# Kernel optimization log

Measured on AMD Instinct MI355X. Metric: run time of the kernel, lower is better.

Reference implementation:

```python
import jax, jax.numpy as jnp
import numpy as np

B, S, D_MODEL, H, D_KV = 2, 2048, 1024, 16, 64
NUM_BUCKETS, MAX_DIST = 32, 128


def _relative_position_bucket(rel_pos, num_buckets=NUM_BUCKETS, max_distance=MAX_DIST):
    # bidirectional (encoder) bucketing, matching T5Attention._relative_position_bucket
    nb = num_buckets // 2
    buckets = (rel_pos > 0).astype(jnp.int32) * nb
    rel = jnp.abs(rel_pos)
    max_exact = nb // 2
    is_small = rel < max_exact
    rel_f = jnp.maximum(rel.astype(jnp.float32), 1.0)  # guard log(0); masked by is_small anyway
    large = max_exact + (
        jnp.log(rel_f / max_exact) / np.log(max_distance / max_exact) * (nb - max_exact)
    ).astype(jnp.int32)
    large = jnp.minimum(large, nb - 1)
    return buckets + jnp.where(is_small, rel, large)


def setup_inputs() -> dict:
    key = jax.random.key(0)
    ks = jax.random.split(key, 6)
    sc = 1.0 / np.sqrt(D_MODEL)
    return {
        "hidden_states": jax.random.normal(ks[0], (B, S, D_MODEL), jnp.float32),
        "Wq": jax.random.normal(ks[1], (D_MODEL, H * D_KV), jnp.float32) * sc,
        "Wk": jax.random.normal(ks[2], (D_MODEL, H * D_KV), jnp.float32) * sc,
        "Wv": jax.random.normal(ks[3], (D_MODEL, H * D_KV), jnp.float32) * sc,
        "Wo": jax.random.normal(ks[4], (H * D_KV, D_MODEL), jnp.float32) * sc,
        "rel_bias_table": jax.random.normal(ks[5], (NUM_BUCKETS, H), jnp.float32),
    }


def reference(hidden_states, Wq, Wk, Wv, Wo, rel_bias_table):
    b, s, _ = hidden_states.shape
    # projections (T5 uses no bias, scale=1.0 in attention)
    q = (hidden_states @ Wq).reshape(b, s, H, D_KV).transpose(0, 2, 1, 3)  # bhsd
    k = (hidden_states @ Wk).reshape(b, s, H, D_KV).transpose(0, 2, 1, 3)
    v = (hidden_states @ Wv).reshape(b, s, H, D_KV).transpose(0, 2, 1, 3)

    # relative position bias: [1, H, S, S]
    ctx = jnp.arange(s)[:, None]
    mem = jnp.arange(s)[None, :]
    buckets = _relative_position_bucket(mem - ctx)          # [S, S]
    pos_bias = rel_bias_table[buckets]                       # [S, S, H]
    pos_bias = pos_bias.transpose(2, 0, 1)[None]             # [1, H, S, S]

    scores = jnp.einsum("bhqd,bhkd->bhqk", q, k) + pos_bias  # scale = 1.0
    probs = jax.nn.softmax(scores, axis=-1)
    attn = jnp.einsum("bhqk,bhkd->bhqd", probs, v)
    attn = attn.transpose(0, 2, 1, 3).reshape(b, s, H * D_KV)
    return attn @ Wo
```

## Files before the change

### kernel.cpp

```cpp
#include <hip/hip_runtime.h>
#include <hip/hip_fp16.h>

#define S_LEN 2048
#define NH 16
#define DK 64
#define DM 1024
#define NB 2
#define QKV_SZ (NB * NH * S_LEN * DK)

typedef _Float16 half8 __attribute__((ext_vector_type(8)));
typedef _Float16 half4v __attribute__((ext_vector_type(4)));
typedef __fp16 fp16x2 __attribute__((ext_vector_type(2)));
typedef float f32x4 __attribute__((ext_vector_type(4)));

static __device__ __forceinline__ half4v pack4(const f32x4 v) {
  fp16x2 lo = __builtin_amdgcn_cvt_pkrtz(v[0], v[1]);
  fp16x2 hi = __builtin_amdgcn_cvt_pkrtz(v[2], v[3]);
  half4v r;
  ((fp16x2*)&r)[0] = lo;
  ((fp16x2*)&r)[1] = hi;
  return r;
}

#define GLL(gp, lp)                                                              \
  __builtin_amdgcn_global_load_lds(                                              \
      (const __attribute__((address_space(1))) unsigned int*)(gp),               \
      (__attribute__((address_space(3))) unsigned int*)(lp), 16, 0, 0)


__global__ __launch_bounds__(256) void conv_f32_f16(const float* __restrict__ in,
                                                    _Float16* __restrict__ out, int n4) {
  int i = blockIdx.x * 256 + threadIdx.x;
  if (i >= n4) return;
  float4 v = ((const float4*)in)[i];
  half4v o;
  o[0] = (_Float16)v.x; o[1] = (_Float16)v.y; o[2] = (_Float16)v.z; o[3] = (_Float16)v.w;
  ((half4v*)out)[i] = o;
}

__global__ __launch_bounds__(256) void transpose_conv4(
    const float* __restrict__ Wq, const float* __restrict__ Wk,
    const float* __restrict__ Wv, const float* __restrict__ Wo,
    _Float16* __restrict__ Wqkvt, _Float16* __restrict__ Wot) {
  __shared__ float tile[32][33];
  int z = blockIdx.z;
  const float* W = (z == 0) ? Wq : (z == 1) ? Wk : (z == 2) ? Wv : Wo;
  _Float16* Wt = (z < 3) ? (Wqkvt + (size_t)z * 1048576) : Wot;
  float scale = (z == 0) ? 1.44269504f : 1.0f;
  int tx = threadIdx.x, ty = threadIdx.y;
  int nx = blockIdx.x * 32 + tx;
  int ky = blockIdx.y * 32;
#pragma unroll
  for (int i = 0; i < 32; i += 8) tile[ty + i][tx] = W[(size_t)(ky + ty + i) * DM + nx];
  __syncthreads();
  int kx = ky + tx;
  int ny = blockIdx.x * 32;
#pragma unroll
  for (int i = 0; i < 32; i += 8)
    Wt[(size_t)(ny + ty + i) * DM + kx] = (_Float16)(tile[tx][ty + i] * scale);
}

__global__ __launch_bounds__(256) void bias_tab_kernel(const float* __restrict__ table,
                                                       float* __restrict__ tab) {
  int i = blockIdx.x * 256 + threadIdx.x;
  if (i >= NH * 4095) return;
  int h = i / 4095, r = i - h * 4095;
  int rel = r - 2047;
  int bucket = rel > 0 ? 16 : 0;
  int a = rel < 0 ? -rel : rel;
  if (a < 8) {
    bucket += a;
  } else {
    int lg = 31 - __clz(a * a);
    int large = 8 + (lg - 6);
    bucket += (large < 15 ? large : 15);
  }
  tab[i] = table[bucket * NH + h] * 1.44269504f;
}

template <int MODE>
__global__ __launch_bounds__(256) void gemm_f16(const _Float16* __restrict__ A,
                                                const _Float16* __restrict__ Bt,
                                                void* __restrict__ Cout,
                                                int M, int N, int K) {
  __shared__ _Float16 As[128 * 32];
  __shared__ _Float16 Bs[128 * 32];
  const int t = threadIdx.x;
  const int m0 = blockIdx.y * 128, n0 = blockIdx.x * 128;
  const int w = t >> 6, lane = t & 63, l15 = lane & 15, quad = lane >> 4;
  const int wr = (w >> 1) * 64, wc = (w & 1) * 64;
  const int swz = (quad ^ (l15 & 3)) * 8;

  f32x4 acc[4][4];
#pragma unroll
  for (int i = 0; i < 4; i++)
#pragma unroll
    for (int j = 0; j < 4; j++) acc[i][j] = (f32x4){0.f, 0.f, 0.f, 0.f};

  for (int k0 = 0; k0 < K; k0 += 32) {
    __syncthreads();
#pragma unroll
    for (int i = 0; i < 2; i++) {
      int id = t + 256 * i;
      int row = id >> 2, c = id & 3;
      int cg = c ^ (row & 3);
      GLL(A + (size_t)(m0 + row) * K + k0 + cg * 8, (char*)As + id * 16);
      GLL(Bt + (size_t)(n0 + row) * K + k0 + cg * 8, (char*)Bs + id * 16);
    }
    __syncthreads();
    half8 af[4], bf[4];
#pragma unroll
    for (int i = 0; i < 4; i++) af[i] = *(const half8*)(As + (wr + i * 16 + l15) * 32 + swz);
#pragma unroll
    for (int i = 0; i < 4; i++) bf[i] = *(const half8*)(Bs + (wc + i * 16 + l15) * 32 + swz);
#pragma unroll
    for (int i = 0; i < 4; i++)
#pragma unroll
      for (int j = 0; j < 4; j++)
        acc[i][j] = __builtin_amdgcn_mfma_f32_16x16x32_f16(af[i], bf[j], acc[i][j], 0, 0, 0);
  }

#pragma unroll
  for (int i = 0; i < 4; i++)
#pragma unroll
    for (int j = 0; j < 4; j++) {
      int row0 = m0 + wr + i * 16 + quad * 4;
      int col = n0 + wc + j * 16 + l15;
      if (MODE == 1) {
#pragma unroll
        for (int r = 0; r < 4; r++)
          ((float*)Cout)[(size_t)(row0 + r) * N + col] = acc[i][j][r];
      } else {
        int which = col >> 10, rem = col & 1023, hh = rem >> 6, dd = rem & 63;
        int bb = row0 >> 11, ss = row0 & 2047;
        _Float16* base = (_Float16*)Cout;
        if (which == 2) {
          *(half4v*)(base + (size_t)2 * QKV_SZ +
                     ((size_t)((bb * NH + hh) * DK + dd)) * S_LEN + ss) = pack4(acc[i][j]);
        } else {
#pragma unroll
          for (int r = 0; r < 4; r++)
            base[(size_t)which * QKV_SZ +
                 ((size_t)((bb * NH + hh) * S_LEN) + ss + r) * DK + dd] = (_Float16)acc[i][j][r];
        }
      }
    }
}

__global__ __launch_bounds__(256, 4) void attn_kernel(
    const _Float16* __restrict__ Q, const _Float16* __restrict__ K,
    const _Float16* __restrict__ Vt, const float* __restrict__ btab,
    _Float16* __restrict__ attn_out) {
  __shared__ _Float16 Ks[4096];
  __shared__ _Float16 Vs[4096];
  __shared__ _Float16 Ps[4][1024];
  __shared__ float slab[512];

  const int t = threadIdx.x;
  const int Q0 = blockIdx.x * 64;
  const int h = blockIdx.y, b = blockIdx.z;
  const int w = t >> 6, lane = t & 63, l15 = lane & 15, quad = lane >> 4;
  const int qw0 = Q0 + w * 16;
  const int sw7 = l15 & 7;

  const _Float16* Qb = Q + (size_t)(b * NH + h) * S_LEN * DK;
  const _Float16* Kb = K + (size_t)(b * NH + h) * S_LEN * DK;
  const _Float16* Vb = Vt + (size_t)(b * NH + h) * S_LEN * DK;

  for (int i = t; i < 512; i += 256) slab[i] = btab[h * 4095 + 1791 + i];

  half8 qf[2];
#pragma unroll
  for (int dh = 0; dh < 2; dh++)
    qf[dh] = *(const half8*)(Qb + (size_t)(qw0 + l15) * DK + dh * 32 + quad * 8);

  f32x4 o[4];
#pragma unroll
  for (int dt = 0; dt < 4; dt++) o[dt] = (f32x4){0.f, 0.f, 0.f, 0.f};
  float m_ = -INFINITY, l_ = 0.f;

  for (int k0 = 0; k0 < S_LEN; k0 += 64) {
#pragma unroll
    for (int i = 0; i < 2; i++) {
      int id = t + 256 * i;
      int row = id >> 3, c = id & 7;
      int cg = c ^ (row & 7);
      GLL(Kb + (size_t)(k0 + row) * DK + cg * 8, (char*)Ks + id * 16);
      GLL(Vb + (size_t)row * S_LEN + k0 + cg * 8, (char*)Vs + id * 16);
    }
    __syncthreads();

    const int dk0 = k0 - qw0;
    const bool farneg = (dk0 <= -191);
    const bool farpos = (dk0 >= 143);
    const bool nearc = !(farneg || farpos);
    const float cb = farneg ? slab[128] : slab[384];

    f32x4 st[4];
    if (nearc) {
#pragma unroll
      for (int kt = 0; kt < 4; kt++) {
        int i0 = dk0 + kt * 16 + quad * 4 - l15 + 256;
        f32x4 v;
        v[0] = slab[i0]; v[1] = slab[i0 + 1]; v[2] = slab[i0 + 2]; v[3] = slab[i0 + 3];
        st[kt] = v;
      }
    } else {
#pragma unroll
      for (int kt = 0; kt < 4; kt++) st[kt] = (f32x4){0.f, 0.f, 0.f, 0.f};
    }

    half8 kf[4][2], vf[4][2];
#pragma unroll
    for (int kt = 0; kt < 4; kt++)
#pragma unroll
      for (int dh = 0; dh < 2; dh++)
        kf[kt][dh] = *(const half8*)(&Ks[(kt * 16 + l15) * 64 + (((dh << 2) + quad) ^ sw7) * 8]);
#pragma unroll
    for (int dt = 0; dt < 4; dt++)
#pragma unroll
      for (int kh = 0; kh < 2; kh++)
        vf[dt][kh] = *(const half8*)(&Vs[(dt * 16 + l15) * 64 + (((kh << 2) + quad) ^ sw7) * 8]);

#pragma unroll
    for (int kt = 0; kt < 4; kt++)
#pragma unroll
      for (int dh = 0; dh < 2; dh++)
        st[kt] = __builtin_amdgcn_mfma_f32_16x16x32_f16(kf[kt][dh], qf[dh], st[kt], 0, 0, 0);

    float cm = fmaxf(fmaxf(st[0][0], st[0][1]), fmaxf(st[0][2], st[0][3]));
#pragma unroll
    for (int kt = 1; kt < 4; kt++)
      cm = fmaxf(cm, fmaxf(fmaxf(st[kt][0], st[kt][1]), fmaxf(st[kt][2], st[kt][3])));
    cm = fmaxf(cm, __shfl_xor(cm, 16));
    cm = fmaxf(cm, __shfl_xor(cm, 32));
    float mc = nearc ? cm : cm + cb;
    if (__any(mc > m_)) {
      float mnew = fmaxf(m_, mc);
      float alpha = __builtin_amdgcn_exp2f(m_ - mnew);
      m_ = mnew;
      l_ *= alpha;
#pragma unroll
      for (int dt = 0; dt < 4; dt++) o[dt] *= alpha;
    }
    float msub = nearc ? m_ : m_ - cb;

    f32x4 lacc = (f32x4){0.f, 0.f, 0.f, 0.f};
#pragma unroll
    for (int kt = 0; kt < 4; kt++) {
      f32x4 p;
#pragma unroll
      for (int r = 0; r < 4; r++) p[r] = __builtin_amdgcn_exp2f(st[kt][r] - msub);
      lacc += p;
      int g = 2 * kt + (quad >> 1);
      *(half4v*)(&Ps[w][l15 * 64 + (g ^ sw7) * 8 + (quad & 1) * 4]) = pack4(p);
    }
    l_ += (lacc[0] + lacc[1]) + (lacc[2] + lacc[3]);
    __asm__ volatile("s_waitcnt lgkmcnt(0)" ::: "memory");

    half8 pf[2];
#pragma unroll
    for (int kh = 0; kh < 2; kh++)
      pf[kh] = *(const half8*)(&Ps[w][l15 * 64 + (((kh << 2) + quad) ^ sw7) * 8]);
#pragma unroll
    for (int dt = 0; dt < 4; dt++)
#pragma unroll
      for (int kh = 0; kh < 2; kh++)
        o[dt] = __builtin_amdgcn_mfma_f32_16x16x32_f16(vf[dt][kh], pf[kh], o[dt], 0, 0, 0);
    __syncthreads();
  }

  float lf = l_;
  lf += __shfl_xor(lf, 16);
  lf += __shfl_xor(lf, 32);
  float inv = 1.0f / lf;
  int q = qw0 + l15;
#pragma unroll
  for (int dt = 0; dt < 4; dt++) {
    f32x4 ov = o[dt] * inv;
    *(half4v*)(attn_out + ((size_t)(b * S_LEN + q)) * DM + h * DK + dt * 16 + quad * 4) =
        pack4(ov);
  }
}

extern "C" void kernel_launch(void* const* d_in, const int* in_sizes, int n_in,
                              void* d_out, int out_size, void* d_ws, size_t ws_size,
                              hipStream_t stream) {
  const float* hs  = (const float*)d_in[0];
  const float* Wq  = (const float*)d_in[1];
  const float* Wk  = (const float*)d_in[2];
  const float* Wv  = (const float*)d_in[3];
  const float* Wo  = (const float*)d_in[4];
  const float* tbl = (const float*)d_in[5];
  float* out = (float*)d_out;
  char* ws = (char*)d_ws;

  _Float16* Xh    = (_Float16*)(ws);
  _Float16* Wqkvt = (_Float16*)(ws + (8u << 20));
  _Float16* Wot   = (_Float16*)(ws + (14u << 20));
  _Float16* Qd    = (_Float16*)(ws + (16u << 20));
  _Float16* Kd    = Qd + (size_t)QKV_SZ;
  _Float16* Vd    = Qd + (size_t)2 * QKV_SZ;
  _Float16* Ah    = (_Float16*)(ws + (40u << 20));
  float*    btab  = (float*)(ws + (48u << 20));

  conv_f32_f16<<<4096, 256, 0, stream>>>(hs, Xh, (NB * S_LEN * DM) / 4);
  transpose_conv4<<<dim3(32, 32, 4), dim3(32, 8), 0, stream>>>(Wq, Wk, Wv, Wo, Wqkvt, Wot);
  bias_tab_kernel<<<256, 256, 0, stream>>>(tbl, btab);

  gemm_f16<0><<<dim3(24, 32), 256, 0, stream>>>(Xh, Wqkvt, (void*)Qd, NB * S_LEN, 3 * DM, DM);
  attn_kernel<<<dim3(S_LEN / 64, NH, NB), 256, 0, stream>>>(Qd, Kd, Vd, btab, Ah);
  gemm_f16<1><<<dim3(8, 32), 256, 0, stream>>>(Ah, Wot, (void*)out, NB * S_LEN, DM, DM);
}
```

Baseline: 218.0 us.

## Double-buffer K/V tiles and process two query subtiles per wave in attention

The attention kernel now prefetches the next K/V tile into a second LDS buffer while the current tile is being processed, so global loads overlap with compute. Each wave handles 32 query rows as two 16-row subtiles, which lets each K/V fragment read from LDS feed two MFMAs. The grid shrinks to 128 queries per block and launch bounds drop to 2 blocks per CU, trading occupancy and more LDS and registers for better reuse and latency hiding. The raw s_barrier calls and manual vmcnt waits must be exactly right for the double buffering to stay correct.

```diff
diff --git a/kernel.cpp b/kernel.cpp
--- a/kernel.cpp
+++ b/kernel.cpp
@@ -147,20 +147,20 @@
     }
 }
 
-__global__ __launch_bounds__(256, 4) void attn_kernel(
+__global__ __launch_bounds__(256, 2) void attn_kernel(
     const _Float16* __restrict__ Q, const _Float16* __restrict__ K,
     const _Float16* __restrict__ Vt, const float* __restrict__ btab,
     _Float16* __restrict__ attn_out) {
-  __shared__ _Float16 Ks[4096];
-  __shared__ _Float16 Vs[4096];
-  __shared__ _Float16 Ps[4][1024];
+  __shared__ _Float16 Ks[2][4096];
+  __shared__ _Float16 Vs[2][4096];
+  __shared__ _Float16 Ps[4][2048];
   __shared__ float slab[512];
 
   const int t = threadIdx.x;
-  const int Q0 = blockIdx.x * 64;
+  const int Q0 = blockIdx.x * 128;
   const int h = blockIdx.y, b = blockIdx.z;
   const int w = t >> 6, lane = t & 63, l15 = lane & 15, quad = lane >> 4;
-  const int qw0 = Q0 + w * 16;
+  const int qw0 = Q0 + w * 32;
   const int sw7 = l15 & 7;
 
   const _Float16* Qb = Q + (size_t)(b * NH + h) * S_LEN * DK;
@@ -169,117 +169,156 @@
 
   for (int i = t; i < 512; i += 256) slab[i] = btab[h * 4095 + 1791 + i];
 
-  half8 qf[2];
-#pragma unroll
-  for (int dh = 0; dh < 2; dh++)
-    qf[dh] = *(const half8*)(Qb + (size_t)(qw0 + l15) * DK + dh * 32 + quad * 8);
-
-  f32x4 o[4];
-#pragma unroll
-  for (int dt = 0; dt < 4; dt++) o[dt] = (f32x4){0.f, 0.f, 0.f, 0.f};
-  float m_ = -INFINITY, l_ = 0.f;
-
+  half8 qf[2][2];
+#pragma unroll
+  for (int u = 0; u < 2; u++)
+#pragma unroll
+    for (int dh = 0; dh < 2; dh++)
+      qf[dh][u] = *(const half8*)(Qb + (size_t)(qw0 + u * 16 + l15) * DK + dh * 32 + quad * 8);
+
+  f32x4 o[4][2];
+#pragma unroll
+  for (int dt = 0; dt < 4; dt++)
+#pragma unroll
+    for (int u = 0; u < 2; u++) o[dt][u] = (f32x4){0.f, 0.f, 0.f, 0.f};
+  float m_[2] = {-INFINITY, -INFINITY}, l_[2] = {0.f, 0.f};
+
+#define STAGE(bs, kk0)                                                           \
+  do {                                                                           \
+    _Pragma("unroll")                                                            \
+    for (int i_ = 0; i_ < 2; i_++) {                                             \
+      int id_ = t + 256 * i_;                                                    \
+      int row_ = id_ >> 3, c_ = id_ & 7, cg_ = c_ ^ (row_ & 7);                  \
+      GLL(Kb + (size_t)((kk0) + row_) * DK + cg_ * 8, (char*)Ks[bs] + id_ * 16); \
+      GLL(Vb + (size_t)row_ * S_LEN + (kk0) + cg_ * 8, (char*)Vs[bs] + id_ * 16);\
+    }                                                                            \
+  } while (0)
+
+  STAGE(0, 0);
+  __asm__ volatile("s_waitcnt vmcnt(0) lgkmcnt(0)" ::: "memory");
+  __builtin_amdgcn_s_barrier();
+
+  int cur = 0;
   for (int k0 = 0; k0 < S_LEN; k0 += 64) {
-#pragma unroll
-    for (int i = 0; i < 2; i++) {
-      int id = t + 256 * i;
-      int row = id >> 3, c = id & 7;
-      int cg = c ^ (row & 7);
-      GLL(Kb + (size_t)(k0 + row) * DK + cg * 8, (char*)Ks + id * 16);
-      GLL(Vb + (size_t)row * S_LEN + k0 + cg * 8, (char*)Vs + id * 16);
-    }
-    __syncthreads();
-
-    const int dk0 = k0 - qw0;
-    const bool farneg = (dk0 <= -191);
-    const bool farpos = (dk0 >= 143);
-    const bool nearc = !(farneg || farpos);
-    const float cb = farneg ? slab[128] : slab[384];
-
-    f32x4 st[4];
-    if (nearc) {
+    if (k0 + 64 < S_LEN) {
+      STAGE(cur ^ 1, k0 + 64);
+      __asm__ volatile("s_waitcnt vmcnt(4)" ::: "memory");
+    } else {
+      __asm__ volatile("s_waitcnt vmcnt(0)" ::: "memory");
+    }
+    __builtin_amdgcn_s_barrier();
+
+    const _Float16* Kc = Ks[cur];
+    const _Float16* Vc = Vs[cur];
+
+    half8 kf[4][2];
+#pragma unroll
+    for (int kt = 0; kt < 4; kt++)
+#pragma unroll
+      for (int dh = 0; dh < 2; dh++)
+        kf[kt][dh] = *(const half8*)(&Kc[(kt * 16 + l15) * 64 + (((dh << 2) + quad) ^ sw7) * 8]);
+
+    f32x4 st[2][4];
+    bool nearc[2];
+    float cb[2];
+#pragma unroll
+    for (int u = 0; u < 2; u++) {
+      const int dk0 = k0 - qw0 - u * 16;
+      const bool farneg = (dk0 <= -191);
+      const bool farpos = (dk0 >= 143);
+      nearc[u] = !(farneg || farpos);
+      cb[u] = farneg ? slab[128] : slab[384];
+      if (nearc[u]) {
+#pragma unroll
+        for (int kt = 0; kt < 4; kt++) {
+          int i0 = dk0 + kt * 16 + quad * 4 - l15 + 256;
+          f32x4 v;
+          v[0] = slab[i0]; v[1] = slab[i0 + 1]; v[2] = slab[i0 + 2]; v[3] = slab[i0 + 3];
+          st[u][kt] = v;
+        }
+      } else {
+#pragma unroll
+        for (int kt = 0; kt < 4; kt++) st[u][kt] = (f32x4){0.f, 0.f, 0.f, 0.f};
+      }
+    }
+
+#pragma unroll
+    for (int kt = 0; kt < 4; kt++)
+#pragma unroll
+      for (int dh = 0; dh < 2; dh++)
+#pragma unroll
+        for (int u = 0; u < 2; u++)
+          st[u][kt] =
+              __builtin_amdgcn_mfma_f32_16x16x32_f16(kf[kt][dh], qf[dh][u], st[u][kt], 0, 0, 0);
+
+#pragma unroll
+    for (int u = 0; u < 2; u++) {
+      float cm = fmaxf(fmaxf(st[u][0][0], st[u][0][1]), fmaxf(st[u][0][2], st[u][0][3]));
+#pragma unroll
+      for (int kt = 1; kt < 4; kt++)
+        cm = fmaxf(cm, fmaxf(fmaxf(st[u][kt][0], st[u][kt][1]), fmaxf(st[u][kt][2], st[u][kt][3])));
+      cm = fmaxf(cm, __shfl_xor(cm, 16));
+      cm = fmaxf(cm, __shfl_xor(cm, 32));
+      float mc = nearc[u] ? cm : cm + cb[u];
+      if (__any(mc > m_[u])) {
+        float mnew = fmaxf(m_[u], mc);
+        float alpha = __builtin_amdgcn_exp2f(m_[u] - mnew);
+        m_[u] = mnew;
+        l_[u] *= alpha;
+#pragma unroll
+        for (int dt = 0; dt < 4; dt++) o[dt][u] *= alpha;
+      }
+      float msub = nearc[u] ? m_[u] : m_[u] - cb[u];
+
+      f32x4 lacc = (f32x4){0.f, 0.f, 0.f, 0.f};
 #pragma unroll
       for (int kt = 0; kt < 4; kt++) {
-        int i0 = dk0 + kt * 16 + quad * 4 - l15 + 256;
-        f32x4 v;
-        v[0] = slab[i0]; v[1] = slab[i0 + 1]; v[2] = slab[i0 + 2]; v[3] = slab[i0 + 3];
-        st[kt] = v;
-      }
-    } else {
-#pragma unroll
-      for (int kt = 0; kt < 4; kt++) st[kt] = (f32x4){0.f, 0.f, 0.f, 0.f};
-    }
-
-    half8 kf[4][2], vf[4][2];
-#pragma unroll
-    for (int kt = 0; kt < 4; kt++)
-#pragma unroll
-      for (int dh = 0; dh < 2; dh++)
-        kf[kt][dh] = *(const half8*)(&Ks[(kt * 16 + l15) * 64 + (((dh << 2) + quad) ^ sw7) * 8]);
+        f32x4 p;
+#pragma unroll
+        for (int r = 0; r < 4; r++) p[r] = __builtin_amdgcn_exp2f(st[u][kt][r] - msub);
+        lacc += p;
+        int g = 2 * kt + (quad >> 1);
+        *(half4v*)(&Ps[w][(u * 16 + l15) * 64 + (g ^ sw7) * 8 + (quad & 1) * 4]) = pack4(p);
+      }
+      l_[u] += (lacc[0] + lacc[1]) + (lacc[2] + lacc[3]);
+    }
+    __asm__ volatile("s_waitcnt lgkmcnt(0)" ::: "memory");
+
+    half8 pf[2][2];
+#pragma unroll
+    for (int kh = 0; kh < 2; kh++)
+#pragma unroll
+      for (int u = 0; u < 2; u++)
+        pf[kh][u] = *(const half8*)(&Ps[w][(u * 16 + l15) * 64 + (((kh << 2) + quad) ^ sw7) * 8]);
+
 #pragma unroll
     for (int dt = 0; dt < 4; dt++)
 #pragma unroll
-      for (int kh = 0; kh < 2; kh++)
-        vf[dt][kh] = *(const half8*)(&Vs[(dt * 16 + l15) * 64 + (((kh << 2) + quad) ^ sw7) * 8]);
-
-#pragma unroll
-    for (int kt = 0; kt < 4; kt++)
-#pragma unroll
-      for (int dh = 0; dh < 2; dh++)
-        st[kt] = __builtin_amdgcn_mfma_f32_16x16x32_f16(kf[kt][dh], qf[dh], st[kt], 0, 0, 0);
-
-    float cm = fmaxf(fmaxf(st[0][0], st[0][1]), fmaxf(st[0][2], st[0][3]));
-#pragma unroll
-    for (int kt = 1; kt < 4; kt++)
-      cm = fmaxf(cm, fmaxf(fmaxf(st[kt][0], st[kt][1]), fmaxf(st[kt][2], st[kt][3])));
-    cm = fmaxf(cm, __shfl_xor(cm, 16));
-    cm = fmaxf(cm, __shfl_xor(cm, 32));
-    float mc = nearc ? cm : cm + cb;
-    if (__any(mc > m_)) {
-      float mnew = fmaxf(m_, mc);
-      float alpha = __builtin_amdgcn_exp2f(m_ - mnew);
-      m_ = mnew;
-      l_ *= alpha;
-#pragma unroll
-      for (int dt = 0; dt < 4; dt++) o[dt] *= alpha;
-    }
-    float msub = nearc ? m_ : m_ - cb;
-
-    f32x4 lacc = (f32x4){0.f, 0.f, 0.f, 0.f};
-#pragma unroll
-    for (int kt = 0; kt < 4; kt++) {
-      f32x4 p;
-#pragma unroll
-      for (int r = 0; r < 4; r++) p[r] = __builtin_amdgcn_exp2f(st[kt][r] - msub);
-      lacc += p;
-      int g = 2 * kt + (quad >> 1);
-      *(half4v*)(&Ps[w][l15 * 64 + (g ^ sw7) * 8 + (quad & 1) * 4]) = pack4(p);
-    }
-    l_ += (lacc[0] + lacc[1]) + (lacc[2] + lacc[3]);
-    __asm__ volatile("s_waitcnt lgkmcnt(0)" ::: "memory");
-
-    half8 pf[2];
-#pragma unroll
-    for (int kh = 0; kh < 2; kh++)
-      pf[kh] = *(const half8*)(&Ps[w][l15 * 64 + (((kh << 2) + quad) ^ sw7) * 8]);
-#pragma unroll
-    for (int dt = 0; dt < 4; dt++)
-#pragma unroll
-      for (int kh = 0; kh < 2; kh++)
-        o[dt] = __builtin_amdgcn_mfma_f32_16x16x32_f16(vf[dt][kh], pf[kh], o[dt], 0, 0, 0);
-    __syncthreads();
+      for (int kh = 0; kh < 2; kh++) {
+        half8 vf = *(const half8*)(&Vc[(dt * 16 + l15) * 64 + (((kh << 2) + quad) ^ sw7) * 8]);
+#pragma unroll
+        for (int u = 0; u < 2; u++)
+          o[dt][u] = __builtin_amdgcn_mfma_f32_16x16x32_f16(vf, pf[kh][u], o[dt][u], 0, 0, 0);
+      }
+
+    __builtin_amdgcn_s_barrier();
+    cur ^= 1;
   }
-
-  float lf = l_;
-  lf += __shfl_xor(lf, 16);
-  lf += __shfl_xor(lf, 32);
-  float inv = 1.0f / lf;
-  int q = qw0 + l15;
-#pragma unroll
-  for (int dt = 0; dt < 4; dt++) {
-    f32x4 ov = o[dt] * inv;
-    *(half4v*)(attn_out + ((size_t)(b * S_LEN + q)) * DM + h * DK + dt * 16 + quad * 4) =
-        pack4(ov);
+#undef STAGE
+
+#pragma unroll
+  for (int u = 0; u < 2; u++) {
+    float lf = l_[u];
+    lf += __shfl_xor(lf, 16);
+    lf += __shfl_xor(lf, 32);
+    float inv = 1.0f / lf;
+    int q = qw0 + u * 16 + l15;
+#pragma unroll
+    for (int dt = 0; dt < 4; dt++) {
+      f32x4 ov = o[dt][u] * inv;
+      *(half4v*)(attn_out + ((size_t)(b * S_LEN + q)) * DM + h * DK + dt * 16 + quad * 4) =
+          pack4(ov);
+    }
   }
 }
 
@@ -309,6 +348,6 @@
   bias_tab_kernel<<<256, 256, 0, stream>>>(tbl, btab);
 
   gemm_f16<0><<<dim3(24, 32), 256, 0, stream>>>(Xh, Wqkvt, (void*)Qd, NB * S_LEN, 3 * DM, DM);
-  attn_kernel<<<dim3(S_LEN / 64, NH, NB), 256, 0, stream>>>(Qd, Kd, Vd, btab, Ah);
+  attn_kernel<<<dim3(S_LEN / 128, NH, NB), 256, 0, stream>>>(Qd, Kd, Vd, btab, Ah);
   gemm_f16<1><<<dim3(8, 32), 256, 0, stream>>>(Ah, Wot, (void*)out, NB * S_LEN, DM, DM);
 }
```

After: 225.7 us. +3.5%, slower.

## Double-buffer K/V tiles and feed P from registers via 16x16x16 MFMA

Applied to the files above, without the earlier changes.

Adds double-buffered LDS for K and V so the next tile's global-to-LDS load is issued before computing on the current tile. This hides load latency and leaves one barrier per iteration. It also drops the per-wave P staging through shared memory: the packed fp16 probabilities stay in registers and feed 16x16x16 MFMAs, whose operand layout matches the QK^T output. The trade-offs are twice the K/V LDS footprint, more MFMA instructions of smaller K, and correctness depending on the async loads being complete before the buffer is read after the barrier.

```diff
diff --git a/kernel.cpp b/kernel.cpp
--- a/kernel.cpp
+++ b/kernel.cpp
@@ -151,9 +151,8 @@
     const _Float16* __restrict__ Q, const _Float16* __restrict__ K,
     const _Float16* __restrict__ Vt, const float* __restrict__ btab,
     _Float16* __restrict__ attn_out) {
-  __shared__ _Float16 Ks[4096];
-  __shared__ _Float16 Vs[4096];
-  __shared__ _Float16 Ps[4][1024];
+  __shared__ _Float16 Ks[2][4096];
+  __shared__ _Float16 Vs[2][4096];
   __shared__ float slab[512];
 
   const int t = threadIdx.x;
@@ -179,16 +178,26 @@
   for (int dt = 0; dt < 4; dt++) o[dt] = (f32x4){0.f, 0.f, 0.f, 0.f};
   float m_ = -INFINITY, l_ = 0.f;
 
+#define STAGE(bs, kk0)                                                           \
+  do {                                                                           \
+    _Pragma("unroll")                                                            \
+    for (int i_ = 0; i_ < 2; i_++) {                                             \
+      int id_ = t + 256 * i_;                                                    \
+      int row_ = id_ >> 3, c_ = id_ & 7, cg_ = c_ ^ (row_ & 7);                  \
+      GLL(Kb + (size_t)((kk0) + row_) * DK + cg_ * 8, (char*)Ks[bs] + id_ * 16); \
+      GLL(Vb + (size_t)row_ * S_LEN + (kk0) + cg_ * 8, (char*)Vs[bs] + id_ * 16);\
+    }                                                                            \
+  } while (0)
+
+  STAGE(0, 0);
+  __syncthreads();
+
+  int cur = 0;
   for (int k0 = 0; k0 < S_LEN; k0 += 64) {
-#pragma unroll
-    for (int i = 0; i < 2; i++) {
-      int id = t + 256 * i;
-      int row = id >> 3, c = id & 7;
-      int cg = c ^ (row & 7);
-      GLL(Kb + (size_t)(k0 + row) * DK + cg * 8, (char*)Ks + id * 16);
-      GLL(Vb + (size_t)row * S_LEN + k0 + cg * 8, (char*)Vs + id * 16);
-    }
-    __syncthreads();
+    if (k0 + 64 < S_LEN) STAGE(cur ^ 1, k0 + 64);
+
+    const _Float16* Kc = Ks[cur];
+    const _Float16* Vc = Vs[cur];
 
     const int dk0 = k0 - qw0;
     const bool farneg = (dk0 <= -191);
@@ -210,17 +219,12 @@
       for (int kt = 0; kt < 4; kt++) st[kt] = (f32x4){0.f, 0.f, 0.f, 0.f};
     }
 
-    half8 kf[4][2], vf[4][2];
+    half8 kf[4][2];
 #pragma unroll
     for (int kt = 0; kt < 4; kt++)
 #pragma unroll
       for (int dh = 0; dh < 2; dh++)
-        kf[kt][dh] = *(const half8*)(&Ks[(kt * 16 + l15) * 64 + (((dh << 2) + quad) ^ sw7) * 8]);
-#pragma unroll
-    for (int dt = 0; dt < 4; dt++)
-#pragma unroll
-      for (int kh = 0; kh < 2; kh++)
-        vf[dt][kh] = *(const half8*)(&Vs[(dt * 16 + l15) * 64 + (((kh << 2) + quad) ^ sw7) * 8]);
+        kf[kt][dh] = *(const half8*)(&Kc[(kt * 16 + l15) * 64 + (((dh << 2) + quad) ^ sw7) * 8]);
 
 #pragma unroll
     for (int kt = 0; kt < 4; kt++)
@@ -245,6 +249,7 @@
     }
     float msub = nearc ? m_ : m_ - cb;
 
+    half4v p16[4];
     f32x4 lacc = (f32x4){0.f, 0.f, 0.f, 0.f};
 #pragma unroll
     for (int kt = 0; kt < 4; kt++) {
@@ -252,23 +257,26 @@
 #pragma unroll
       for (int r = 0; r < 4; r++) p[r] = __builtin_amdgcn_exp2f(st[kt][r] - msub);
       lacc += p;
-      int g = 2 * kt + (quad >> 1);
-      *(half4v*)(&Ps[w][l15 * 64 + (g ^ sw7) * 8 + (quad & 1) * 4]) = pack4(p);
+      p16[kt] = pack4(p);
     }
     l_ += (lacc[0] + lacc[1]) + (lacc[2] + lacc[3]);
-    __asm__ volatile("s_waitcnt lgkmcnt(0)" ::: "memory");
-
-    half8 pf[2];
-#pragma unroll
-    for (int kh = 0; kh < 2; kh++)
-      pf[kh] = *(const half8*)(&Ps[w][l15 * 64 + (((kh << 2) + quad) ^ sw7) * 8]);
-#pragma unroll
-    for (int dt = 0; dt < 4; dt++)
-#pragma unroll
-      for (int kh = 0; kh < 2; kh++)
-        o[dt] = __builtin_amdgcn_mfma_f32_16x16x32_f16(vf[dt][kh], pf[kh], o[dt], 0, 0, 0);
+
+#pragma unroll
+    for (int dt = 0; dt < 4; dt++) {
+      half4v vf[4];
+#pragma unroll
+      for (int kt = 0; kt < 4; kt++)
+        vf[kt] = *(const half4v*)(&Vc[(dt * 16 + l15) * 64 +
+                                      ((2 * kt + (quad >> 1)) ^ sw7) * 8 + (quad & 1) * 4]);
+#pragma unroll
+      for (int kt = 0; kt < 4; kt++)
+        o[dt] = __builtin_amdgcn_mfma_f32_16x16x16f16(vf[kt], p16[kt], o[dt], 0, 0, 0);
+    }
+
     __syncthreads();
+    cur ^= 1;
   }
+#undef STAGE
 
   float lf = l_;
   lf += __shfl_xor(lf, 16);
```

Measured after the change: 220.3 us. About the same (+1.0%).
